# Kernel tuning notes

Hardware: AMD Instinct MI355X
Metric: run time of the kernel (lower is better)

## Reference

```python
import jax, jax.numpy as jnp
import numpy as np

Y0 = 0.28209479177387814  # real spherical harmonic Y_0^0 = 1/(2*sqrt(pi))
KSIZE = 5
PAD = 2


def _radial_masks(kernel_size):
    """Binary masks, one per distinct squared radius in the kernel grid (matches
    _compute_spherical_coords_and_masks: voxels sharing r^2 share a mask)."""
    c = (kernel_size - 1) // 2
    g = np.arange(kernel_size) - c
    ii, jj, kk = np.meshgrid(g, g, g, indexing='ij')
    r2 = ii ** 2 + jj ** 2 + kk ** 2
    vals = np.unique(r2)
    return np.stack([(r2 == v).astype(np.float32) for v in vals], axis=0)  # [P,K,K,K]


def setup_inputs() -> dict:
    key = jax.random.key(0)
    k1, k2, k3 = jax.random.split(key, 3)
    masks = jnp.asarray(_radial_masks(KSIZE))              # [P=10, 5, 5, 5]
    P = masks.shape[0]
    x = jax.random.normal(k1, (2, 32, 1, 48, 48, 48), dtype=jnp.float32)
    weight = jax.random.normal(k2, (64, 32, 1, 1, 1, P), dtype=jnp.float32)
    bias = 0.1 * jax.random.normal(k3, (64,), dtype=jnp.float32)
    return {"x": x, "weight": weight, "bias": bias, "masks": masks}


def reference(x, weight, bias, masks):
    B, I = x.shape[0], x.shape[1]
    O = weight.shape[0]
    # Filter build (order_in=order_out=order_filter=1): CG_000 = 1, Y_0 constant.
    # F[o,i,x,y,z] = Y0 * sum_p W[o,i,p] * mask[p,x,y,z]
    filt = Y0 * jnp.einsum('oip,pxyz->oixyz', weight[:, :, 0, 0, 0, :], masks)
    xr = x.reshape(B, I * x.shape[2], *x.shape[3:])        # [B, I, D, H, W]
    out = jax.lax.conv_general_dilated(
        xr, filt, window_strides=(1, 1, 1), padding=[(PAD, PAD)] * 3,
        dimension_numbers=('NCDHW', 'OIDHW', 'NCDHW'))
    out = out.reshape(B, O, 1, *out.shape[2:])             # [B, O, 1, D, H, W]
    # bias added only to the l=0 irrep channel (index 0 of dim 2; size 1 here)
    return out + bias[None, :, None, None, None, None]
```

## Files before the change

### kernel.cpp

```cpp
#include <hip/hip_runtime.h>
#include <stdint.h>

#define V3 110592
#define PLANE 2304
#define NO 64

typedef unsigned short ushort_t;
typedef __attribute__((ext_vector_type(8))) short short8v;
typedef __attribute__((ext_vector_type(4))) float float4v;

__device__ __forceinline__ uint32_t f2bf1(float f) {
  uint32_t u = __float_as_uint(f);
  u += 0x7FFFu + ((u >> 16) & 1u);
  return u >> 16;
}
__device__ __forceinline__ uint32_t pack2(float a, float b) {
  return f2bf1(a) | (f2bf1(b) << 16);
}

__global__ void prep_kernel(const float* __restrict__ w, ushort_t* __restrict__ Afr) {
  int idx = blockIdx.x * 256 + threadIdx.x;
  if (idx >= 120 * 64 * 8) return;
  int r = idx & 7, m = (idx >> 3) & 63, g = idx >> 9;
  int kk = g * 8 + r;
  int dzi = kk / 192, k2 = kk % 192;
  int i = k2 / 6, qi = k2 % 6;
  const int Q[6] = {0, 1, 2, 4, 5, 8};
  const int pidx[13] = {0, 1, 2, 3, 4, 5, 6, 0, 7, 8, 0, 0, 9};
  int dz = dzi - 2;
  int p = pidx[Q[qi] + dz * dz];
  Afr[idx] = (ushort_t)f2bf1(0.28209479177387814f * w[(m * 32 + i) * 10 + p]);
}

__global__ __launch_bounds__(256, 4) void bq_kernel(const float* __restrict__ x,
                                                    ushort_t* __restrict__ Bq) {
  const int tid = threadIdx.x;
  const int lane = tid & 63;
  const int strip = tid >> 6;
  const int d = blockIdx.x;
  const int ig = blockIdx.y & 7;
  const int half = blockIdx.y >> 3;
  const float* xb = x + (size_t)blockIdx.z * 32 * V3;
  ushort_t* Bqb = Bq + (size_t)blockIdx.z * ((size_t)1152 * PLANE * 8);

  const int h0 = (half * 4 + strip) * 6;
  const int gw = lane - 2;
  const bool okw = (gw >= 0 && gw < 48);
  const int sl1 = lane > 0 ? lane - 1 : 0;
  const int sl2 = lane > 1 ? lane - 2 : 0;
  const int sr1 = lane < 63 ? lane + 1 : 63;
  const int sr2 = lane < 62 ? lane + 2 : 63;
  const bool okst = (lane >= 2 && lane <= 49);

  const float* px[4];
#pragma unroll
  for (int ii = 0; ii < 4; ++ii)
    px[ii] = xb + ((size_t)(ig * 4 + ii) * 48 + d) * PLANE + gw;

  float v[10][4];
#pragma unroll
  for (int r = 0; r < 10; ++r) {
    const int gh = h0 - 2 + r;
    const bool okv = okw && (gh >= 0) && (gh < 48);
#pragma unroll
    for (int ii = 0; ii < 4; ++ii)
      v[r][ii] = okv ? px[ii][gh * 48] : 0.f;
  }

  float s1[4][5], s4[4][5];
#pragma unroll
  for (int r = 0; r < 10; ++r) {
    const int slot = r % 5;
#pragma unroll
    for (int ii = 0; ii < 4; ++ii) {
      float val = v[r][ii];
      float vl1 = __shfl(val, sl1);
      float vr1 = __shfl(val, sr1);
      float vl2 = __shfl(val, sl2);
      float vr2 = __shfl(val, sr2);
      s1[ii][slot] = vl1 + vr1;
      s4[ii][slot] = vl2 + vr2;
    }
    if (r >= 4) {
      const int j0 = (r - 4) % 5, j1 = (r - 3) % 5, j2 = (r - 2) % 5,
                j3 = (r - 1) % 5, j4 = r % 5;
      uint32_t dw[12];
#pragma unroll
      for (int ii = 0; ii < 4; ++ii) {
        float B0 = v[r - 2][ii];
        float B1 = s1[ii][j2] + v[r - 3][ii] + v[r - 1][ii];
        float B2 = s1[ii][j1] + s1[ii][j3];
        float B3 = s4[ii][j2] + v[r - 4][ii] + v[r][ii];
        float B4 = s4[ii][j1] + s4[ii][j3] + s1[ii][j0] + s1[ii][j4];
        float B5 = s4[ii][j0] + s4[ii][j4];
        dw[ii * 3 + 0] = pack2(B0, B1);
        dw[ii * 3 + 1] = pack2(B2, B3);
        dw[ii * 3 + 2] = pack2(B4, B5);
      }
      if (okst) {
        const int n = (h0 + r - 4) * 48 + gw;
        const size_t gb = (size_t)(d * 24 + ig * 3);
        uint4 c0 = {dw[0], dw[1], dw[2], dw[3]};
        uint4 c1 = {dw[4], dw[5], dw[6], dw[7]};
        uint4 c2 = {dw[8], dw[9], dw[10], dw[11]};
        *(uint4*)(Bqb + ((gb + 0) * PLANE + n) * 8) = c0;
        *(uint4*)(Bqb + ((gb + 1) * PLANE + n) * 8) = c1;
        *(uint4*)(Bqb + ((gb + 2) * PLANE + n) * 8) = c2;
      }
    }
  }
}

__global__ __launch_bounds__(256, 4) void gemm_kernel(const ushort_t* __restrict__ Bq,
                                                      const ushort_t* __restrict__ Afr,
                                                      const float* __restrict__ bias,
                                                      float* __restrict__ out) {
  const int tid = threadIdx.x;
  const int lane = tid & 63, wi = tid >> 6;
  const int quad = lane >> 4, m15 = lane & 15;
  const int b = blockIdx.x;
  const int p = b & 7;
  const int s = b >> 3;
  const int dl = s / 9;
  const int nbl = s - dl * 9;
  const int d = (p >> 1) * 12 + dl;
  const int n0 = ((p & 1) * 9 + nbl) * 128 + wi * 32;
  const ushort_t* Bqb = Bq + (size_t)blockIdx.z * ((size_t)1152 * PLANE * 8);
  float* outb = out + (size_t)blockIdx.z * (size_t)NO * V3;

  const int lo = (d < 2) ? (2 - d) : 0;
  const int hi = (d > 45) ? (49 - d) : 4;
  const int kslo = 6 * lo;
  const int T = 6 * (hi - lo + 1);

  const ushort_t* ap = Afr + ((size_t)(kslo * 4 + quad) * 64 + m15) * 8;
  const ushort_t* bp = Bqb + ((size_t)((d - 2) * 24 + kslo * 4 + quad) * PLANE + n0 + m15) * 8;
  const int astep = 4 * 64 * 8;
  const int bstep = 4 * PLANE * 8;

  float4v acc[4][2];
#pragma unroll
  for (int mt = 0; mt < 4; ++mt)
#pragma unroll
    for (int nt = 0; nt < 2; ++nt) acc[mt][nt] = (float4v){0.f, 0.f, 0.f, 0.f};

  short8v A0[4], B0[2], A1[4], B1[2], A2[4], B2[2];

#define SBAR __builtin_amdgcn_sched_barrier(0)
#define LOADSET(Ax, Bx)                                                        \
  {                                                                            \
    _Pragma("unroll") for (int nt = 0; nt < 2; ++nt)                           \
        Bx[nt] = *(const short8v*)(bp + nt * 128);                             \
    _Pragma("unroll") for (int mt = 0; mt < 4; ++mt)                           \
        Ax[mt] = *(const short8v*)(ap + mt * 128);                             \
    ap += astep; bp += bstep;                                                  \
  }
#define MFMASET(Ax, Bx)                                                        \
  {                                                                            \
    __builtin_amdgcn_s_setprio(1);                                             \
    _Pragma("unroll") for (int mt = 0; mt < 4; ++mt)                           \
        _Pragma("unroll") for (int nt = 0; nt < 2; ++nt)                       \
            acc[mt][nt] = __builtin_amdgcn_mfma_f32_16x16x32_bf16(             \
                Ax[mt], Bx[nt], acc[mt][nt], 0, 0, 0);                         \
    __builtin_amdgcn_s_setprio(0);                                             \
  }

  LOADSET(A0, B0);
  LOADSET(A1, B1);
  SBAR;
  for (int k = 0; k < T - 3; k += 3) {
    LOADSET(A2, B2); SBAR;
    MFMASET(A0, B0); SBAR;
    LOADSET(A0, B0); SBAR;
    MFMASET(A1, B1); SBAR;
    LOADSET(A1, B1); SBAR;
    MFMASET(A2, B2); SBAR;
  }
  LOADSET(A2, B2); SBAR;
  MFMASET(A0, B0);
  MFMASET(A1, B1);
  MFMASET(A2, B2);
#undef LOADSET
#undef MFMASET
#undef SBAR

  const int vb = d * PLANE + n0 + m15;
#pragma unroll
  for (int mt = 0; mt < 4; ++mt) {
#pragma unroll
    for (int r = 0; r < 4; ++r) {
      int m = mt * 16 + quad * 4 + r;
      float bv = bias[m];
      float* op = outb + (size_t)m * V3 + vb;
#pragma unroll
      for (int nt = 0; nt < 2; ++nt)
        op[nt * 16] = acc[mt][nt][r] + bv;
    }
  }
}

extern "C" void kernel_launch(void* const* d_in, const int* in_sizes, int n_in,
                              void* d_out, int out_size, void* d_ws, size_t ws_size,
                              hipStream_t stream) {
  const float* x    = (const float*)d_in[0];
  const float* w    = (const float*)d_in[1];
  const float* bias = (const float*)d_in[2];
  float* out = (float*)d_out;

  ushort_t* Afr = (ushort_t*)d_ws;
  ushort_t* Bq  = (ushort_t*)((char*)d_ws + 131072);
  const size_t SB = (size_t)1152 * PLANE * 8 * 2;
  const bool both = (ws_size >= 131072 + 2 * SB);

  prep_kernel<<<240, 256, 0, stream>>>(w, Afr);
  if (both) {
    bq_kernel<<<dim3(48, 16, 2), 256, 0, stream>>>(x, Bq);
    gemm_kernel<<<dim3(864, 1, 2), 256, 0, stream>>>(Bq, Afr, bias, out);
  } else {
    for (int b = 0; b < 2; ++b) {
      bq_kernel<<<dim3(48, 16, 1), 256, 0, stream>>>(x + (size_t)b * 32 * V3, Bq);
      gemm_kernel<<<dim3(864, 1, 1), 256, 0, stream>>>(Bq, Afr, bias,
                                                       out + (size_t)b * NO * V3);
    }
  }
}
```

Measured before the change: 150.3 us.

## Fold weight prep into bq kernel, remap blocks to match gemm, nontemporal output stores

Removes the separate prep_kernel launch by having the first 240 blocks of bq_kernel also build the bf16 filter fragments. bq_kernel moves to a 1D grid whose block-to-(depth, half, channel group) mapping mirrors the gemm kernel's depth-group interleave, which may improve cache locality between producer and consumer. The gemm output stores become nontemporal to avoid polluting cache with the large fp32 output. The fallback path passes zbase 0 for both batch iterations, so prep runs twice there, which is redundant but harmless.

```diff
diff --git a/kernel.cpp b/kernel.cpp
--- a/kernel.cpp
+++ b/kernel.cpp
@@ -18,9 +18,8 @@
   return f2bf1(a) | (f2bf1(b) << 16);
 }
 
-__global__ void prep_kernel(const float* __restrict__ w, ushort_t* __restrict__ Afr) {
-  int idx = blockIdx.x * 256 + threadIdx.x;
-  if (idx >= 120 * 64 * 8) return;
+__device__ __forceinline__ void prep_body(const float* __restrict__ w,
+                                          ushort_t* __restrict__ Afr, int idx) {
   int r = idx & 7, m = (idx >> 3) & 63, g = idx >> 9;
   int kk = g * 8 + r;
   int dzi = kk / 192, k2 = kk % 192;
@@ -33,15 +32,26 @@
 }
 
 __global__ __launch_bounds__(256, 4) void bq_kernel(const float* __restrict__ x,
-                                                    ushort_t* __restrict__ Bq) {
+                                                    ushort_t* __restrict__ Bq,
+                                                    const float* __restrict__ w,
+                                                    ushort_t* __restrict__ Afr,
+                                                    int zbase) {
   const int tid = threadIdx.x;
+  const int b = blockIdx.x;
+  if (zbase == 0 && b < 240) prep_body(w, Afr, b * 256 + tid);
+
+  const int q = b & 7;
+  const int dg = q >> 1, half = q & 1;
+  const int s = b >> 3;
+  const int dl = s % 12;
+  const int ig = (s / 12) & 7;
+  const int z = zbase + s / 96;
+  const int d = dg * 12 + dl;
+
   const int lane = tid & 63;
   const int strip = tid >> 6;
-  const int d = blockIdx.x;
-  const int ig = blockIdx.y & 7;
-  const int half = blockIdx.y >> 3;
-  const float* xb = x + (size_t)blockIdx.z * 32 * V3;
-  ushort_t* Bqb = Bq + (size_t)blockIdx.z * ((size_t)1152 * PLANE * 8);
+  const float* xb = x + (size_t)z * 32 * V3;
+  ushort_t* Bqb = Bq + (size_t)z * ((size_t)1152 * PLANE * 8);
 
   const int h0 = (half * 4 + strip) * 6;
   const int gw = lane - 2;
@@ -194,7 +204,7 @@
       float* op = outb + (size_t)m * V3 + vb;
 #pragma unroll
       for (int nt = 0; nt < 2; ++nt)
-        op[nt * 16] = acc[mt][nt][r] + bv;
+        __builtin_nontemporal_store(acc[mt][nt][r] + bv, op + nt * 16);
     }
   }
 }
@@ -212,13 +222,12 @@
   const size_t SB = (size_t)1152 * PLANE * 8 * 2;
   const bool both = (ws_size >= 131072 + 2 * SB);
 
-  prep_kernel<<<240, 256, 0, stream>>>(w, Afr);
   if (both) {
-    bq_kernel<<<dim3(48, 16, 2), 256, 0, stream>>>(x, Bq);
+    bq_kernel<<<dim3(1536), 256, 0, stream>>>(x, Bq, w, Afr, 0);
     gemm_kernel<<<dim3(864, 1, 2), 256, 0, stream>>>(Bq, Afr, bias, out);
   } else {
     for (int b = 0; b < 2; ++b) {
-      bq_kernel<<<dim3(48, 16, 1), 256, 0, stream>>>(x + (size_t)b * 32 * V3, Bq);
+      bq_kernel<<<dim3(768), 256, 0, stream>>>(x + (size_t)b * 32 * V3, Bq, w, Afr, 0);
       gemm_kernel<<<dim3(864, 1, 1), 256, 0, stream>>>(Bq, Afr, bias,
                                                        out + (size_t)b * NO * V3);
     }
```

New measurement: 149.0 us. About the same (-0.9%).
